# Optimization experiments

Hardware: AMD Instinct MI355X
Metric: run time of the kernel (lower is better)

The kernel has to match this reference:

```python
import jax, jax.numpy as jnp
import numpy as np
import math

L_SIDE = 32           # one_side_length = ceil(sqrt(L)), L = 32**2
NDIM = 16             # args.ndim (SSM state size)
N_SSM = 16            # args.n_ssm
DIRS = 4              # args.directions_amount
EMBED = 1024          # embed_dim
KD = DIRS * N_SSM     # kernel_dim = 64
CDIM = EMBED * DIRS   # C_dimensions = 4096
H = EMBED // N_SSM    # 64 (channels per ssm)
R2 = 16               # expansion terms per kernel position
R = L_SIDE * L_SIDE * R2
V = 2 * L_SIDE        # vander power dim (power_dim = kernel_dim_arg*2)
BSZ = 8
SEQ = L_SIDE * L_SIDE


def _build_one_matrix():
    # Mimics CoeffCalculator.whole_as_one: for each of d=2 flow axes and each
    # of R expansion terms, the 4 A-factor rows are one-hot selectors over the
    # V power basis, and the 5th (B) row holds an integer coefficient in one of
    # the first two columns (selecting B1 or B2).
    rng = np.random.default_rng(0)
    M = np.zeros((2, 5, R, V), dtype=np.float32)
    di = np.arange(2)[:, None]
    ri = np.arange(R)[None, :]
    for a in range(4):
        idx = rng.integers(0, V, size=(2, R))
        M[di, a, ri, idx] = 1.0
    col = rng.integers(0, 2, size=(2, R))
    coef = rng.integers(1, 5, size=(2, R)).astype(np.float32)
    M[di, 4, ri, col] = coef
    return jnp.asarray(M)


def setup_inputs() -> dict:
    key = jax.random.key(0)
    ks = jax.random.split(key, 7)
    return {
        "x": jax.random.normal(ks[0], (SEQ, BSZ, EMBED), jnp.float32),
        "A": jax.random.normal(ks[1], (4, KD, NDIM), jnp.float32) * 0.2,
        "B1": jax.random.normal(ks[2], (KD, NDIM), jnp.float32) * 0.2,
        "B2": jax.random.normal(ks[3], (KD, NDIM), jnp.float32) * 0.2,
        "C1": jax.random.normal(ks[4], (CDIM, NDIM), jnp.float32),
        "C2": jax.random.normal(ks[5], (CDIM, NDIM), jnp.float32),
        "omega": jax.random.normal(ks[6], (EMBED,), jnp.float32),
        "one_matrix": _build_one_matrix(),
    }


def _compute_kernel(A, B1, B2, C1, C2, one_matrix, dtype):
    scale = 1.0 / math.sqrt(NDIM)
    # _calc_coeffs: sigmoid on A, B
    As = jax.nn.sigmoid(A)                                  # (4, KD, NDIM)
    pw = jnp.arange(V, dtype=dtype)
    # torch.linalg.vander: increasing powers 0..V-1 -> (4, V, KD, NDIM)
    A_vals = jnp.transpose(As[..., None] ** pw, (0, 3, 1, 2))
    Bs = jax.nn.sigmoid(jnp.stack([B1, B2], 0))             # (2, KD, NDIM)
    Bpad = jnp.zeros((V, KD, NDIM), dtype).at[:2].set(Bs)   # pad to V rows
    vals = jnp.concatenate([A_vals, Bpad[None]], 0)         # (5, V, KD, NDIM)
    # 'd a R V, a V k n -> d a R k n' then product over the 5 factors
    prod = jnp.einsum('drv,vkn->drkn', one_matrix[:, 0], vals[0])
    for a in range(1, 5):
        prod = prod * jnp.einsum('drv,vkn->drkn', one_matrix[:, a], vals[a])
    # sum over r2 expansion terms per kernel position
    w = prod.reshape(2, SEQ, R2, KD, NDIM).sum(2)           # (2, SEQ, KD, NDIM)
    C = jnp.stack([C1, C2], 0) * scale                      # (2, CDIM, NDIM)
    Cr = C.reshape(2, H, KD, NDIM)
    k = jnp.einsum('dpkn,dhkn->phk', w, Cr).reshape(L_SIDE, L_SIDE, CDIM)
    # boundary scaling (first row/col x2, corner net x1)
    k = k.at[0, :, :].multiply(2.0)
    k = k.at[:, 0, :].multiply(2.0)
    k = k.at[0, 0, :].divide(4.0)
    return k


def reference(x, A, B1, B2, C1, C2, omega, one_matrix):
    k = _compute_kernel(A, B1, B2, C1, C2, one_matrix, x.dtype)
    # channel layout (H, dir, n_ssm) -> per-direction (EMBED,) kernels
    kd = k.reshape(L_SIDE, L_SIDE, H, DIRS, N_SSM)
    kd = jnp.transpose(kd, (3, 2, 4, 0, 1)).reshape(DIRS, EMBED, L_SIDE, L_SIDE)
    # 4-corner scans: flip kernel per direction; conv is linear so sum kernels
    ksum = kd[0] + kd[1, :, ::-1, :] + kd[2, :, :, ::-1] + kd[3, :, ::-1, ::-1]
    residual = x * omega                                    # 'L B D, D -> L B D'
    xg = jnp.transpose(x, (1, 2, 0)).reshape(BSZ, EMBED, L_SIDE, L_SIDE)
    s = 2 * L_SIDE
    xf = jnp.fft.rfft2(xg, s=(s, s))                        # (B, D, s, s//2+1)
    kf = jnp.fft.rfft2(ksum, s=(s, s))
    y = jnp.fft.irfft2(xf * kf, s=(s, s))[..., :L_SIDE, :L_SIDE]
    y = jnp.transpose(y.reshape(BSZ, EMBED, SEQ), (2, 0, 1))  # back to (L, B, D)
    return y + residual
```

## Files before the change

### kernel.cpp

```cpp
#include <hip/hip_runtime.h>
#include <stdint.h>


typedef __attribute__((ext_vector_type(8))) short short8;
typedef __attribute__((ext_vector_type(4))) float f32x4;

__device__ inline uint16_t f2bf(float f) {
    uint32_t u = __float_as_uint(f);
    uint32_t r = (u + 0x7FFFu + ((u >> 16) & 1u)) >> 16;
    return (uint16_t)r;
}
__device__ inline float bf2f(uint16_t v) {
    return __uint_as_float((uint32_t)v << 16);
}
__device__ inline uint32_t packbf(float a, float b) {
    return (uint32_t)f2bf(a) | ((uint32_t)f2bf(b) << 16);
}

__global__ __launch_bounds__(256) void k_pre(const float* __restrict__ x,
                                             uint16_t* __restrict__ xtb,
                                             const float* __restrict__ A,
                                             const float* __restrict__ B1,
                                             const float* __restrict__ B2,
                                             float* __restrict__ LAg,
                                             float* __restrict__ SBg) {
    __shared__ __align__(16) float shf[32 * 129];
    int bx = blockIdx.x;
    int t = threadIdx.x;

    if (bx < 2048) {
        int u = bx & 31, e0 = ((bx >> 5) & 31) * 32, r0 = (bx >> 10) * 128;
        {
            int c = t & 7, a = t >> 3;
            const float* src = x + (size_t)(u * 256 + r0) * 1024 + e0 + c * 4;
            #pragma unroll
            for (int qq = 0; qq < 4; ++qq) {
                int r = qq * 32 + a;
                float4 v = *(const float4*)(src + (size_t)r * 1024);
                shf[(c * 4 + 0) * 129 + r] = v.x;
                shf[(c * 4 + 1) * 129 + r] = v.y;
                shf[(c * 4 + 2) * 129 + r] = v.z;
                shf[(c * 4 + 3) * 129 + r] = v.w;
            }
        }
        __syncthreads();
        {
            int e_local = t >> 3, b = t & 7;
            const float* row = shf + e_local * 129;
            int v0 = r0 >> 3;
            uint32_t pk[8];
            #pragma unroll
            for (int k2 = 0; k2 < 8; ++k2)
                pk[k2] = packbf(row[(2 * k2) * 8 + b], row[(2 * k2 + 1) * 8 + b]);
            uint16_t* dst = xtb + (size_t)(e0 + e_local) * 8192 + u * 256 + b * 32 + v0;
            *(uint4*)dst       = make_uint4(pk[0], pk[1], pk[2], pk[3]);
            *(uint4*)(dst + 8) = make_uint4(pk[4], pk[5], pk[6], pk[7]);
        }
    } else {
        int i = bx - 2048;
        int e = t * 4;
        if (i < 4) {
            float4 v = *(const float4*)(A + i * 1024 + e);
            float4 o;
            o.x = -log2f(1.0f + expf(-v.x));
            o.y = -log2f(1.0f + expf(-v.y));
            o.z = -log2f(1.0f + expf(-v.z));
            o.w = -log2f(1.0f + expf(-v.w));
            *(float4*)(LAg + i * 1024 + e) = o;
        } else {
            const float* Bs = (i == 4) ? B1 : B2;
            float4 v = *(const float4*)(Bs + e);
            float4 o;
            o.x = 1.0f / (1.0f + expf(-v.x));
            o.y = 1.0f / (1.0f + expf(-v.y));
            o.z = 1.0f / (1.0f + expf(-v.z));
            o.w = 1.0f / (1.0f + expf(-v.w));
            *(float4*)(SBg + (i - 4) * 1024 + e) = o;
        }
    }
}

__global__ __launch_bounds__(256) void k_w(const float* __restrict__ om,
                                           const float* __restrict__ LAg,
                                           const float* __restrict__ SBg,
                                           float* __restrict__ w) {
    __shared__ float ffl[16][4];
    __shared__ float cfl[16][2];
    int bx = blockIdx.x;
    int d = bx >> 10, p = bx & 1023;
    int t = threadIdx.x;
    {
        int row_id = t >> 2, h = t & 3;
        int a = row_id >> 4, r2 = row_id & 15;
        const float* src = om + ((size_t)(d * 5 + a) * 16384 + p * 16 + r2) * 64 + h * 16;
        float s = 0.0f;
        #pragma unroll
        for (int q = 0; q < 4; ++q) {
            float4 v = *(const float4*)(src + q * 4);
            float jb = (float)(h * 16 + q * 4);
            s = __builtin_fmaf(v.x, jb,
                __builtin_fmaf(v.y, jb + 1.0f,
                __builtin_fmaf(v.z, jb + 2.0f,
                __builtin_fmaf(v.w, jb + 3.0f, s))));
        }
        s += __shfl_xor(s, 1);
        s += __shfl_xor(s, 2);
        if (h == 0) ffl[r2][a] = s;
        if (t < 16) {
            const float* c = om + ((size_t)(d * 5 + 4) * 16384 + p * 16 + t) * 64;
            cfl[t][0] = c[0];
            cfl[t][1] = c[1];
        }
    }
    __syncthreads();

    int j0 = t * 4;
    float L0[4], L1[4], L2[4], L3[4], B0v[4], B1v[4], acc[4];
    #pragma unroll
    for (int a = 0; a < 4; ++a) {
        float* La = (a == 0) ? L0 : (a == 1) ? L1 : (a == 2) ? L2 : L3;
        float4 u0 = *(const float4*)(LAg + a * 1024 + j0);
        La[0] = u0.x; La[1] = u0.y; La[2] = u0.z; La[3] = u0.w;
    }
    {
        float4 u0 = *(const float4*)(SBg + j0);
        float4 v0 = *(const float4*)(SBg + 1024 + j0);
        B0v[0] = u0.x; B0v[1] = u0.y; B0v[2] = u0.z; B0v[3] = u0.w;
        B1v[0] = v0.x; B1v[1] = v0.y; B1v[2] = v0.z; B1v[3] = v0.w;
    }
    #pragma unroll
    for (int jj = 0; jj < 4; ++jj) acc[jj] = 0.0f;

    #pragma unroll
    for (int r2 = 0; r2 < 16; ++r2) {
        float f0 = ffl[r2][0];
        float f1 = ffl[r2][1];
        float f2 = ffl[r2][2];
        float f3 = ffl[r2][3];
        float c0 = cfl[r2][0];
        float c1 = cfl[r2][1];
        #pragma unroll
        for (int jj = 0; jj < 4; ++jj) {
            float ex = __builtin_fmaf(f3, L3[jj],
                       __builtin_fmaf(f2, L2[jj],
                       __builtin_fmaf(f1, L1[jj], f0 * L0[jj])));
            float bs = __builtin_fmaf(c1, B1v[jj], c0 * B0v[jj]);
            acc[jj] = __builtin_fmaf(exp2f(ex), bs, acc[jj]);
        }
    }
    float* dst = w + (size_t)(d * 1024 + p) * 1024 + j0;
    *(float4*)dst = make_float4(acc[0], acc[1], acc[2], acc[3]);
}

__global__ __launch_bounds__(256) void k_kd(const float* __restrict__ w,
                                            const float* __restrict__ C1,
                                            const float* __restrict__ C2,
                                            uint16_t* __restrict__ kd4b) {
    __shared__ float Wl[128 * 33];
    __shared__ float Ctl[32 * 65];
    int kap = blockIdx.x;
    int p0 = blockIdx.y * 128;
    int dir = kap >> 4, m = kap & 15;
    int t = threadIdx.x;

    {
        int off = (t & 3) * 4;
        #pragma unroll
        for (int rep = 0; rep < 4; ++rep) {
            int row_id = rep * 64 + (t >> 2);
            int d = row_id >> 7, pp = row_id & 127;
            const float* src = w + ((size_t)(d * 1024 + p0 + pp) * 64 + kap) * 16 + off;
            float4 v = *(const float4*)src;
            float* dstl = Wl + pp * 33 + d * 16 + off;
            dstl[0] = v.x; dstl[1] = v.y; dstl[2] = v.z; dstl[3] = v.w;
        }
    }
    if (t < 128) {
        int d = t >> 6, h = t & 63;
        const float* Cd = d ? C2 : C1;
        const float* src = Cd + (size_t)(h * 64 + kap) * 16;
        #pragma unroll
        for (int q = 0; q < 16; ++q)
            Ctl[(d * 16 + q) * 65 + h] = src[q] * 0.25f;
    }
    __syncthreads();

    int ph = t & 15, hq = t >> 4;
    int pl = ph * 8, h0 = hq * 4;
    float acc[8][4];
    #pragma unroll
    for (int i = 0; i < 8; ++i)
        { acc[i][0] = acc[i][1] = acc[i][2] = acc[i][3] = 0.0f; }

    for (int k = 0; k < 32; ++k) {
        float c0 = Ctl[k * 65 + h0 + 0];
        float c1 = Ctl[k * 65 + h0 + 1];
        float c2 = Ctl[k * 65 + h0 + 2];
        float c3 = Ctl[k * 65 + h0 + 3];
        #pragma unroll
        for (int i = 0; i < 8; ++i) {
            float wv = Wl[(pl + i) * 33 + k];
            acc[i][0] += wv * c0; acc[i][1] += wv * c1;
            acc[i][2] += wv * c2; acc[i][3] += wv * c3;
        }
    }
    #pragma unroll
    for (int j = 0; j < 4; ++j) {
        int h = h0 + j;
        uint32_t pk[4];
        #pragma unroll
        for (int qq = 0; qq < 4; ++qq) {
            float v0, v1;
            #pragma unroll
            for (int z = 0; z < 2; ++z) {
                int p = p0 + pl + qq * 2 + z;
                int ii = p >> 5, jj = p & 31;
                float f = ((ii == 0) != (jj == 0)) ? 2.0f : 1.0f;
                float val = acc[qq * 2 + z][j] * f;
                if (z == 0) v0 = val; else v1 = val;
            }
            pk[qq] = packbf(v0, v1);
        }
        uint16_t* dst = kd4b + ((size_t)(dir * 1024 + h * 16 + m)) * 1024 + p0 + pl;
        *(uint4*)dst = make_uint4(pk[0], pk[1], pk[2], pk[3]);
    }
}

__global__ __launch_bounds__(256) void k_conv(const uint16_t* __restrict__ xtb,
                                              const uint16_t* __restrict__ kd4b,
                                              uint16_t* __restrict__ ytb) {
    __shared__ __align__(16) char smem[24576 + 16384];
    const int KROW = 768;
    const int SROW = 96;
    char* xtl = smem + 24576;

    int e = blockIdx.x;
    int t = threadIdx.x;
    int lane = t & 63, wv = t >> 6;
    int n = lane & 15, q = lane >> 4, nn = n & 7, hi = n >> 3;

    {
        f32x4 z = {0.f, 0.f, 0.f, 0.f};
        #pragma unroll
        for (int k = 0; k < 6; ++k)
            *(f32x4*)(smem + (t + k * 256) * 16) = z;
    }
    {
        const uint4* src = (const uint4*)(xtb + (size_t)e * 8192);
        #pragma unroll
        for (int r = 0; r < 4; ++r) {
            uint4 v = src[r * 256 + t];
            *(uint4*)(xtl + (r * 256 + t) * 16) = v;
        }
    }
    int pi = t >> 3, pj = (t & 7) * 4;
    float s0, s1, s2, s3;
    {
        const uint16_t* b0 = kd4b + (size_t)e * 1024;
        ushort4 a0 = *(const ushort4*)(b0 + pi * 32 + pj);
        ushort4 a1 = *(const ushort4*)(b0 + (1 << 20) + (31 - pi) * 32 + pj);
        ushort4 a2 = *(const ushort4*)(b0 + (2 << 20) + pi * 32 + (28 - pj));
        ushort4 a3 = *(const ushort4*)(b0 + (3 << 20) + (31 - pi) * 32 + (28 - pj));
        s0 = bf2f(a0.x) + bf2f(a1.x) + bf2f(a2.w) + bf2f(a3.w);
        s1 = bf2f(a0.y) + bf2f(a1.y) + bf2f(a2.z) + bf2f(a3.z);
        s2 = bf2f(a0.z) + bf2f(a1.z) + bf2f(a2.y) + bf2f(a3.y);
        s3 = bf2f(a0.w) + bf2f(a1.w) + bf2f(a2.x) + bf2f(a3.x);
    }
    __syncthreads();

    {
        uint16_t k0 = f2bf(s0), k1 = f2bf(s1), k2 = f2bf(s2), k3 = f2bf(s3);
        #pragma unroll
        for (int s = 0; s < 8; ++s) {
            uint16_t* row = (uint16_t*)(smem + pi * KROW + s * SROW);
            int c = 31 + s - pj;
            row[c]     = k0;
            row[c - 1] = k1;
            row[c - 2] = k2;
            row[c - 3] = k3;
        }
    }
    __syncthreads();

    int A0 = n - 8 * q;
    int A1 = A0 + 16;
    int sh1 = (A1 + 9) & 7;
    int off1 = sh1 * SROW + (31 + sh1 - A1) * 2;
    int off0;
    if (A0 >= -8) {
        int sh0 = (A0 + 9) & 7;
        off0 = sh0 * SROW + (31 + sh0 - A0) * 2;
    } else {
        off0 = 80;
    }
    int boff = nn * 64 + q * 16;
    const char* zptr = smem + 80;

    f32x4 acc0[4], acc1[4];
    #pragma unroll
    for (int ii = 0; ii < 4; ++ii) {
        acc0[ii] = (f32x4){0.f, 0.f, 0.f, 0.f};
        acc1[ii] = (f32x4){0.f, 0.f, 0.f, 0.f};
    }

    #pragma unroll
    for (int j = 0; j < 8; ++j) {
        if (j <= 2 * wv + 1) {
            const char* krow = smem + j * KROW;
            short8 a0 = *(const short8*)(krow + off0);
            short8 a1 = *(const short8*)(krow + off1);
            {
                int u = 2 * wv + hi - j;
                const char* bp = (u >= 0) ? (xtl + u * 512 + boff) : zptr;
                short8 bb = *(const short8*)bp;
                acc0[0] = __builtin_amdgcn_mfma_f32_16x16x32_bf16(a0, bb, acc0[0], 0, 0, 0);
                acc1[0] = __builtin_amdgcn_mfma_f32_16x16x32_bf16(a1, bb, acc1[0], 0, 0, 0);
            }
            #pragma unroll
            for (int ii = 1; ii < 4; ++ii) {
                int u = 2 * wv + 8 * ii + hi - j;
                short8 bb = *(const short8*)(xtl + u * 512 + boff);
                acc0[ii] = __builtin_amdgcn_mfma_f32_16x16x32_bf16(a0, bb, acc0[ii], 0, 0, 0);
                acc1[ii] = __builtin_amdgcn_mfma_f32_16x16x32_bf16(a1, bb, acc1[ii], 0, 0, 0);
            }
        }
    }
    #pragma unroll
    for (int b = 1; b <= 3; ++b) {
        #pragma unroll
        for (int m = 0; m < 8; ++m) {
            int di = 2 * wv + 8 * b - 6 + m;
            const char* krow = smem + di * KROW;
            short8 a0 = *(const short8*)(krow + off0);
            short8 a1 = *(const short8*)(krow + off1);
            #pragma unroll
            for (int ii = b; ii < 4; ++ii) {
                int u = 8 * (ii - b) + 6 + hi - m;
                const char* bp = ((ii == b) && (m == 7) && (hi == 0))
                                     ? zptr : (xtl + u * 512 + boff);
                short8 bb = *(const short8*)bp;
                acc0[ii] = __builtin_amdgcn_mfma_f32_16x16x32_bf16(a0, bb, acc0[ii], 0, 0, 0);
                acc1[ii] = __builtin_amdgcn_mfma_f32_16x16x32_bf16(a1, bb, acc1[ii], 0, 0, 0);
            }
        }
    }

    {
        uint16_t* base = ytb + ((size_t)(nn * 1024 + e)) * 1024 + q * 4;
        #pragma unroll
        for (int ii = 0; ii < 4; ++ii) {
            int ro = 2 * wv + 8 * ii + hi;
            uint2 w0 = make_uint2(packbf(acc0[ii][0], acc0[ii][1]),
                                  packbf(acc0[ii][2], acc0[ii][3]));
            uint2 w1 = make_uint2(packbf(acc1[ii][0], acc1[ii][1]),
                                  packbf(acc1[ii][2], acc1[ii][3]));
            *(uint2*)(base + ro * 32)      = w0;
            *(uint2*)(base + ro * 32 + 16) = w1;
        }
    }
}

__global__ __launch_bounds__(256) void k_t2(const uint16_t* __restrict__ ytb,
                                            const float* __restrict__ x,
                                            const float* __restrict__ omega,
                                            float* __restrict__ out) {
    __shared__ float lds[32 * 130];
    int e0 = blockIdx.x * 32, p0 = blockIdx.y * 128, b = blockIdx.z;
    int t = threadIdx.x;
    {
        int a = t >> 3, c = t & 7;
        const uint16_t* src = ytb + (size_t)(b * 1024 + e0 + a) * 1024 + p0;
        float* dst = lds + a * 130;
        #pragma unroll
        for (int rep = 0; rep < 2; ++rep) {
            int off = (c + rep * 8) * 8;
            uint4 v = *(const uint4*)(src + off);
            uint32_t ww[4] = {v.x, v.y, v.z, v.w};
            #pragma unroll
            for (int k = 0; k < 4; ++k) {
                float2 f;
                f.x = bf2f((uint16_t)(ww[k] & 0xFFFFu));
                f.y = bf2f((uint16_t)(ww[k] >> 16));
                *(float2*)(dst + off + k * 2) = f;
            }
        }
    }
    __syncthreads();
    int pl = t >> 1, eh = (t & 1) * 16;
    int p = p0 + pl;
    const float* xs = x + ((size_t)(p * 8 + b)) * 1024 + e0 + eh;
    float* os = out + ((size_t)(p * 8 + b)) * 1024 + e0 + eh;
    #pragma unroll
    for (int qq = 0; qq < 4; ++qq) {
        float4 xv = *(const float4*)(xs + qq * 4);
        int eb = eh + qq * 4;
        float4 ov;
        ov.x = lds[(eb + 0) * 130 + pl] + xv.x * omega[e0 + eb + 0];
        ov.y = lds[(eb + 1) * 130 + pl] + xv.y * omega[e0 + eb + 1];
        ov.z = lds[(eb + 2) * 130 + pl] + xv.z * omega[e0 + eb + 2];
        ov.w = lds[(eb + 3) * 130 + pl] + xv.w * omega[e0 + eb + 3];
        *(float4*)(os + qq * 4) = ov;
    }
}

extern "C" void kernel_launch(void* const* d_in, const int* in_sizes, int n_in,
                              void* d_out, int out_size, void* d_ws, size_t ws_size,
                              hipStream_t stream) {
    (void)in_sizes; (void)n_in; (void)out_size; (void)ws_size;
    const float* x   = (const float*)d_in[0];
    const float* A   = (const float*)d_in[1];
    const float* B1  = (const float*)d_in[2];
    const float* B2  = (const float*)d_in[3];
    const float* C1  = (const float*)d_in[4];
    const float* C2  = (const float*)d_in[5];
    const float* omg = (const float*)d_in[6];
    const float* om  = (const float*)d_in[7];
    float* out = (float*)d_out;

    float* ws  = (float*)d_ws;
    uint16_t* xtb  = (uint16_t*)ws;
    uint16_t* kd4b = (uint16_t*)(ws + 4194304);
    uint16_t* ytb  = (uint16_t*)(ws + 6291456);
    float* w       = ws + 10485760;
    float* LAg     = ws + 4194304 + 65536;
    float* SBg     = ws + 4194304 + 69632;

    k_pre <<<2054, 256, 0, stream>>>(x, xtb, A, B1, B2, LAg, SBg);
    k_w   <<<2048, 256, 0, stream>>>(om, LAg, SBg, w);
    k_kd  <<<dim3(64, 8), 256, 0, stream>>>(w, C1, C2, kd4b);
    k_conv<<<1024, 256, 0, stream>>>(xtb, kd4b, ytb);
    k_t2  <<<dim3(32, 8, 8), 256, 0, stream>>>(ytb, x, omg, out);
}
```

Baseline: 184.7 us.

## Fuse x transpose and w-coefficient kernels into one interleaved launch

Merges the x-transpose/bf16 pack kernel and the w-coefficient kernel into a single launch. Even blocks do the transpose and odd blocks compute w. Each w block now recomputes the log-sigmoid of A and the sigmoid of B in registers using fast hardware exp2/log2/rcp intrinsics, so the LAg/SBg intermediate buffers and one kernel launch are gone. Interleaving mixes memory-bound transpose blocks with exp-heavy w blocks so they can overlap. The cost is redundant sigmoid work in every w block and slightly less accurate approximate intrinsics.

```diff
diff --git a/kernel.cpp b/kernel.cpp
--- a/kernel.cpp
+++ b/kernel.cpp
@@ -17,19 +17,21 @@
     return (uint32_t)f2bf(a) | ((uint32_t)f2bf(b) << 16);
 }
 
-__global__ __launch_bounds__(256) void k_pre(const float* __restrict__ x,
-                                             uint16_t* __restrict__ xtb,
-                                             const float* __restrict__ A,
-                                             const float* __restrict__ B1,
-                                             const float* __restrict__ B2,
-                                             float* __restrict__ LAg,
-                                             float* __restrict__ SBg) {
+__global__ __launch_bounds__(256) void k_front4(const float* __restrict__ x,
+                                                uint16_t* __restrict__ xtb,
+                                                const float* __restrict__ om,
+                                                const float* __restrict__ A,
+                                                const float* __restrict__ B1,
+                                                const float* __restrict__ B2,
+                                                float* __restrict__ w) {
     __shared__ __align__(16) float shf[32 * 129];
+    const float LOG2E = 1.44269504088896f;
     int bx = blockIdx.x;
     int t = threadIdx.x;
 
-    if (bx < 2048) {
-        int u = bx & 31, e0 = ((bx >> 5) & 31) * 32, r0 = (bx >> 10) * 128;
+    if ((bx & 1) == 0) {
+        int tidx = bx >> 1;
+        int u = tidx & 31, e0 = ((tidx >> 5) & 31) * 32, r0 = (tidx >> 10) * 128;
         {
             int c = t & 7, a = t >> 3;
             const float* src = x + (size_t)(u * 256 + r0) * 1024 + e0 + c * 4;
@@ -57,99 +59,82 @@
             *(uint4*)(dst + 8) = make_uint4(pk[4], pk[5], pk[6], pk[7]);
         }
     } else {
-        int i = bx - 2048;
-        int e = t * 4;
-        if (i < 4) {
-            float4 v = *(const float4*)(A + i * 1024 + e);
-            float4 o;
-            o.x = -log2f(1.0f + expf(-v.x));
-            o.y = -log2f(1.0f + expf(-v.y));
-            o.z = -log2f(1.0f + expf(-v.z));
-            o.w = -log2f(1.0f + expf(-v.w));
-            *(float4*)(LAg + i * 1024 + e) = o;
-        } else {
-            const float* Bs = (i == 4) ? B1 : B2;
-            float4 v = *(const float4*)(Bs + e);
-            float4 o;
-            o.x = 1.0f / (1.0f + expf(-v.x));
-            o.y = 1.0f / (1.0f + expf(-v.y));
-            o.z = 1.0f / (1.0f + expf(-v.z));
-            o.w = 1.0f / (1.0f + expf(-v.w));
-            *(float4*)(SBg + (i - 4) * 1024 + e) = o;
-        }
-    }
-}
-
-__global__ __launch_bounds__(256) void k_w(const float* __restrict__ om,
-                                           const float* __restrict__ LAg,
-                                           const float* __restrict__ SBg,
-                                           float* __restrict__ w) {
-    __shared__ float ffl[16][4];
-    __shared__ float cfl[16][2];
-    int bx = blockIdx.x;
-    int d = bx >> 10, p = bx & 1023;
-    int t = threadIdx.x;
-    {
-        int row_id = t >> 2, h = t & 3;
-        int a = row_id >> 4, r2 = row_id & 15;
-        const float* src = om + ((size_t)(d * 5 + a) * 16384 + p * 16 + r2) * 64 + h * 16;
-        float s = 0.0f;
-        #pragma unroll
-        for (int q = 0; q < 4; ++q) {
-            float4 v = *(const float4*)(src + q * 4);
-            float jb = (float)(h * 16 + q * 4);
-            s = __builtin_fmaf(v.x, jb,
-                __builtin_fmaf(v.y, jb + 1.0f,
-                __builtin_fmaf(v.z, jb + 2.0f,
-                __builtin_fmaf(v.w, jb + 3.0f, s))));
-        }
-        s += __shfl_xor(s, 1);
-        s += __shfl_xor(s, 2);
-        if (h == 0) ffl[r2][a] = s;
-        if (t < 16) {
-            const float* c = om + ((size_t)(d * 5 + 4) * 16384 + p * 16 + t) * 64;
-            cfl[t][0] = c[0];
-            cfl[t][1] = c[1];
-        }
-    }
-    __syncthreads();
-
-    int j0 = t * 4;
-    float L0[4], L1[4], L2[4], L3[4], B0v[4], B1v[4], acc[4];
-    #pragma unroll
-    for (int a = 0; a < 4; ++a) {
-        float* La = (a == 0) ? L0 : (a == 1) ? L1 : (a == 2) ? L2 : L3;
-        float4 u0 = *(const float4*)(LAg + a * 1024 + j0);
-        La[0] = u0.x; La[1] = u0.y; La[2] = u0.z; La[3] = u0.w;
-    }
-    {
-        float4 u0 = *(const float4*)(SBg + j0);
-        float4 v0 = *(const float4*)(SBg + 1024 + j0);
-        B0v[0] = u0.x; B0v[1] = u0.y; B0v[2] = u0.z; B0v[3] = u0.w;
-        B1v[0] = v0.x; B1v[1] = v0.y; B1v[2] = v0.z; B1v[3] = v0.w;
-    }
-    #pragma unroll
-    for (int jj = 0; jj < 4; ++jj) acc[jj] = 0.0f;
-
-    #pragma unroll
-    for (int r2 = 0; r2 < 16; ++r2) {
-        float f0 = ffl[r2][0];
-        float f1 = ffl[r2][1];
-        float f2 = ffl[r2][2];
-        float f3 = ffl[r2][3];
-        float c0 = cfl[r2][0];
-        float c1 = cfl[r2][1];
-        #pragma unroll
-        for (int jj = 0; jj < 4; ++jj) {
-            float ex = __builtin_fmaf(f3, L3[jj],
-                       __builtin_fmaf(f2, L2[jj],
-                       __builtin_fmaf(f1, L1[jj], f0 * L0[jj])));
-            float bs = __builtin_fmaf(c1, B1v[jj], c0 * B0v[jj]);
-            acc[jj] = __builtin_fmaf(exp2f(ex), bs, acc[jj]);
-        }
-    }
-    float* dst = w + (size_t)(d * 1024 + p) * 1024 + j0;
-    *(float4*)dst = make_float4(acc[0], acc[1], acc[2], acc[3]);
+        int wid = bx >> 1;
+        int d = wid >> 10, p = wid & 1023;
+        float* ffl = shf;
+        float* cfl = shf + 64;
+        {
+            int row_id = t >> 2, h = t & 3;
+            int a = row_id >> 4, r2 = row_id & 15;
+            const float* src = om + ((size_t)(d * 5 + a) * 16384 + p * 16 + r2) * 64 + h * 16;
+            float s = 0.0f;
+            #pragma unroll
+            for (int q = 0; q < 4; ++q) {
+                float4 v = *(const float4*)(src + q * 4);
+                float jb = (float)(h * 16 + q * 4);
+                s = __builtin_fmaf(v.x, jb,
+                    __builtin_fmaf(v.y, jb + 1.0f,
+                    __builtin_fmaf(v.z, jb + 2.0f,
+                    __builtin_fmaf(v.w, jb + 3.0f, s))));
+            }
+            s += __shfl_xor(s, 1);
+            s += __shfl_xor(s, 2);
+            if (h == 0) ffl[r2 * 4 + a] = s;
+            if (t < 16) {
+                const float* c = om + ((size_t)(d * 5 + 4) * 16384 + p * 16 + t) * 64;
+                cfl[t * 2 + 0] = c[0];
+                cfl[t * 2 + 1] = c[1];
+            }
+        }
+
+        int j0 = t * 4;
+        float L0[4], L1[4], L2[4], L3[4], B0v[4], B1v[4], acc[4];
+        #pragma unroll
+        for (int a = 0; a < 4; ++a) {
+            float* La = (a == 0) ? L0 : (a == 1) ? L1 : (a == 2) ? L2 : L3;
+            float4 v = *(const float4*)(A + a * 1024 + j0);
+            float tv[4] = {v.x, v.y, v.z, v.w};
+            #pragma unroll
+            for (int k = 0; k < 4; ++k) {
+                float ex = __builtin_amdgcn_exp2f(-tv[k] * LOG2E);
+                La[k] = -__builtin_amdgcn_logf(1.0f + ex);
+            }
+        }
+        {
+            float4 u0 = *(const float4*)(B1 + j0);
+            float4 v0 = *(const float4*)(B2 + j0);
+            float t1v[4] = {u0.x, u0.y, u0.z, u0.w};
+            float t2v[4] = {v0.x, v0.y, v0.z, v0.w};
+            #pragma unroll
+            for (int k = 0; k < 4; ++k) {
+                B0v[k] = __builtin_amdgcn_rcpf(1.0f + __builtin_amdgcn_exp2f(-t1v[k] * LOG2E));
+                B1v[k] = __builtin_amdgcn_rcpf(1.0f + __builtin_amdgcn_exp2f(-t2v[k] * LOG2E));
+            }
+        }
+        #pragma unroll
+        for (int jj = 0; jj < 4; ++jj) acc[jj] = 0.0f;
+        __syncthreads();
+
+        #pragma unroll
+        for (int r2 = 0; r2 < 16; ++r2) {
+            float f0 = ffl[r2 * 4 + 0];
+            float f1 = ffl[r2 * 4 + 1];
+            float f2 = ffl[r2 * 4 + 2];
+            float f3 = ffl[r2 * 4 + 3];
+            float c0 = cfl[r2 * 2 + 0];
+            float c1 = cfl[r2 * 2 + 1];
+            #pragma unroll
+            for (int jj = 0; jj < 4; ++jj) {
+                float ex = __builtin_fmaf(f3, L3[jj],
+                           __builtin_fmaf(f2, L2[jj],
+                           __builtin_fmaf(f1, L1[jj], f0 * L0[jj])));
+                float bs = __builtin_fmaf(c1, B1v[jj], c0 * B0v[jj]);
+                acc[jj] = __builtin_fmaf(exp2f(ex), bs, acc[jj]);
+            }
+        }
+        float* dst = w + (size_t)(d * 1024 + p) * 1024 + j0;
+        *(float4*)dst = make_float4(acc[0], acc[1], acc[2], acc[3]);
+    }
 }
 
 __global__ __launch_bounds__(256) void k_kd(const float* __restrict__ w,
@@ -422,12 +407,9 @@
     uint16_t* kd4b = (uint16_t*)(ws + 4194304);
     uint16_t* ytb  = (uint16_t*)(ws + 6291456);
     float* w       = ws + 10485760;
-    float* LAg     = ws + 4194304 + 65536;
-    float* SBg     = ws + 4194304 + 69632;
-
-    k_pre <<<2054, 256, 0, stream>>>(x, xtb, A, B1, B2, LAg, SBg);
-    k_w   <<<2048, 256, 0, stream>>>(om, LAg, SBg, w);
-    k_kd  <<<dim3(64, 8), 256, 0, stream>>>(w, C1, C2, kd4b);
-    k_conv<<<1024, 256, 0, stream>>>(xtb, kd4b, ytb);
-    k_t2  <<<dim3(32, 8, 8), 256, 0, stream>>>(ytb, x, omg, out);
-}
+
+    k_front4<<<4096, 256, 0, stream>>>(x, xtb, om, A, B1, B2, w);
+    k_kd    <<<dim3(64, 8), 256, 0, stream>>>(w, C1, C2, kd4b);
+    k_conv  <<<1024, 256, 0, stream>>>(xtb, kd4b, ytb);
+    k_t2    <<<dim3(32, 8, 8), 256, 0, stream>>>(ytb, x, omg, out);
+}
```

Result: no change. 181.6 us (-1.7%).
